# Performance work log

Measured on AMD Instinct MI355X. Metric: run time of the kernel, lower is better.

The kernel has to match this reference:

```python
import jax, jax.numpy as jnp
import numpy as np

N = 50000        # nodes
E = 800000       # edges (before self-loops)
F_IN = 256       # input feature dim
HID = 64         # hidden per head (concat=False -> head mean)
NCLS = 40        # classes
HEADS = 8
NEG_SLOPE = 0.2  # PyG GATConv default leaky_relu slope


def setup_inputs() -> dict:
    key = jax.random.key(0)
    ks = jax.random.split(key, 11)
    s = 0.1
    return {
        "x": jax.random.normal(ks[0], (N, F_IN), jnp.float32),
        "edge_index": jax.random.randint(ks[1], (2, E), 0, N, dtype=jnp.int64),
        "edge_attr": jax.random.uniform(ks[2], (E, 1), jnp.float32),
        "W0": jax.random.normal(ks[3], (HEADS * HID, F_IN), jnp.float32) * s,
        "a0s": jax.random.normal(ks[4], (HEADS, HID), jnp.float32) * s,
        "a0d": jax.random.normal(ks[5], (HEADS, HID), jnp.float32) * s,
        "b0": jnp.zeros((HID,), jnp.float32),
        "W2": jax.random.normal(ks[6], (HEADS * NCLS, HID), jnp.float32) * s,
        "a2s": jax.random.normal(ks[7], (HEADS, NCLS), jnp.float32) * s,
        "a2d": jax.random.normal(ks[8], (HEADS, NCLS), jnp.float32) * s,
        "b2": jnp.zeros((NCLS,), jnp.float32),
    }


def _gat_conv(x, src, dst, W, att_src, att_dst, bias, heads, out_c):
    # Linear: [N, in] @ [heads*out, in]^T -> [N, heads, out]
    h = (x @ W.T).reshape(N, heads, out_c)
    # Per-node attention logits, gathered per edge.
    a_s = jnp.einsum('nhc,hc->nh', h, att_src)
    a_d = jnp.einsum('nhc,hc->nh', h, att_dst)
    e = jax.nn.leaky_relu(a_s[src] + a_d[dst], NEG_SLOPE)  # [E, H]
    # Segment softmax over incoming edges of each destination node.
    m = jax.ops.segment_max(e, dst, num_segments=N)
    p = jnp.exp(e - m[dst])
    denom = jax.ops.segment_sum(p, dst, num_segments=N)
    alpha = p / (denom[dst] + 1e-16)
    # Weighted message scatter-sum: [E,H,C] -> [N,H,C]
    out = jax.ops.segment_sum(alpha[:, :, None] * h[src], dst, num_segments=N)
    # concat=False -> mean over heads, then bias.
    return out.mean(axis=1) + bias


def reference(x, edge_index, edge_attr, W0, a0s, a0d, b0, W2, a2s, a2d, b2):
    # edge_attr is unpacked by the torch forward but never used by GATConv.
    # PyG GATConv adds self-loops by default.
    loops = jnp.arange(N, dtype=edge_index.dtype)
    src = jnp.concatenate([edge_index[0], loops])
    dst = jnp.concatenate([edge_index[1], loops])
    h = jax.nn.relu(_gat_conv(x, src, dst, W0, a0s, a0d, b0, HEADS, HID))
    # dropout is identity in eval mode
    out = _gat_conv(h, src, dst, W2, a2s, a2d, b2, HEADS, NCLS)
    return jax.nn.log_softmax(out, axis=1)
```

## Files before the change

### kernel.cpp

```cpp
#include <hip/hip_runtime.h>
#include <hip/hip_bf16.h>
#include <math.h>


#define NEG_SLOPE 0.2f

typedef short v8s __attribute__((ext_vector_type(8)));
typedef float v4f __attribute__((ext_vector_type(4)));
typedef float v2f __attribute__((ext_vector_type(2)));
typedef unsigned short u16;
typedef unsigned int u32;
typedef unsigned char u8;

__device__ __forceinline__ u16 f2bf(float f) {
    union { float f; u32 u; } v; v.f = f;
    u32 r = v.u + 0x7fffu + ((v.u >> 16) & 1u);
    return (u16)(r >> 16);
}
__device__ __forceinline__ float lrelu_exp(float e) {
    e = (e > 0.f) ? e : NEG_SLOPE * e;
    return __expf(e);
}
__device__ __forceinline__ void dec8(uint2 r, float* h) {
    v2f a = __builtin_amdgcn_cvt_pk_f32_fp8(r.x, false);
    v2f b = __builtin_amdgcn_cvt_pk_f32_fp8(r.x, true);
    v2f c = __builtin_amdgcn_cvt_pk_f32_fp8(r.y, false);
    v2f d = __builtin_amdgcn_cvt_pk_f32_fp8(r.y, true);
    h[0] = a.x; h[1] = a.y; h[2] = b.x; h[3] = b.y;
    h[4] = c.x; h[5] = c.y; h[6] = d.x; h[7] = d.y;
}
__device__ __forceinline__ u8 enc8(float v) {
    u32 p = __builtin_amdgcn_cvt_pk_fp8_f32(v, v, 0u, false);
    return (u8)(p & 0xffu);
}


__global__ __launch_bounds__(256) void histcast_k(const int* __restrict__ ei, int* __restrict__ deg,
                                                  int E, int Nn, int NBh,
                                                  const float* __restrict__ x, u16* __restrict__ xb,
                                                  const float* __restrict__ W0, u16* __restrict__ W0b,
                                                  const float* __restrict__ W2, u16* __restrict__ W2b,
                                                  int nx, int n0c, int n2c) {
    int b = blockIdx.x;
    if (b < NBh) {
        int e = b * 256 + threadIdx.x;
        int ET = E + Nn;
        if (e >= ET) return;
        int d = (e < E) ? ei[E + e] : (e - E);
        atomicAdd(&deg[d], 1);
    } else {
        int i = ((b - NBh) * 256 + threadIdx.x) * 4;
        const float* in; u16* out;
        if (i < nx)            { in = x;  out = xb; }
        else if (i < nx + n0c) { in = W0; out = W0b; i -= nx; }
        else if (i < nx + n0c + n2c) { in = W2; out = W2b; i -= nx + n0c; }
        else return;
        float4 v = *reinterpret_cast<const float4*>(in + i);
        ushort4 o;
        o.x = f2bf(v.x); o.y = f2bf(v.y); o.z = f2bf(v.z); o.w = f2bf(v.w);
        *reinterpret_cast<ushort4*>(out + i) = o;
    }
}


__global__ __launch_bounds__(1024) void scanA_k(const int* __restrict__ deg, int* __restrict__ incl,
                                                int* __restrict__ bsum, int* __restrict__ dbin, int n) {
    __shared__ int wsum[16];
    __shared__ int dh[256];
    int t = threadIdx.x;
    if (t < 256) dh[t] = 0;
    int i = blockIdx.x * 1024 + t;
    int v = (i < n) ? deg[i] : 0;
    __syncthreads();
    if (i < n) atomicAdd(&dh[v < 255 ? v : 255], 1);
    int lane = t & 63, wid = t >> 6;
    int sv = v;
    for (int off = 1; off < 64; off <<= 1) {
        int u = __shfl_up(sv, off, 64);
        if (lane >= off) sv += u;
    }
    if (lane == 63) wsum[wid] = sv;
    __syncthreads();
    if (t < 16) {
        int w = wsum[t];
        for (int off = 1; off < 16; off <<= 1) {
            int u = __shfl_up(w, off, 64);
            if (t >= off) w += u;
        }
        wsum[t] = w;
    }
    if (t < 256 && dh[t] > 0) atomicAdd(&dbin[t], dh[t]);
    __syncthreads();
    int pre = (wid > 0) ? wsum[wid - 1] : 0;
    int inc = pre + sv;
    if (i < n) incl[i] = inc;
    if (t == 1023) bsum[blockIdx.x] = inc;
}


__global__ __launch_bounds__(256) void scanBC_k(const int* __restrict__ incl, const int* __restrict__ deg,
                                                const int* __restrict__ bsum, int* __restrict__ rowstart,
                                                int n, int B) {
    __shared__ int sb[65];
    int t = threadIdx.x;
    if (t < 64) {
        int v = (t < B) ? bsum[t] : 0;
        int sv = v;
        for (int off = 1; off < 64; off <<= 1) {
            int u = __shfl_up(sv, off, 64);
            if (t >= off) sv += u;
        }
        sb[t] = sv - v;
        if (t == 63) sb[64] = sv;
    }
    __syncthreads();
    int i = blockIdx.x * 256 + t;
    if (i < n) rowstart[i] = sb[i >> 10] + incl[i] - deg[i];
    if (i == 0) rowstart[n] = sb[64];
}


__global__ __launch_bounds__(256) void scatter_k(const int* __restrict__ ei,
                                                 const int* __restrict__ rowstart,
                                                 int* __restrict__ cursor,
                                                 int* __restrict__ srcs, int E, int Nn,
                                                 const int* __restrict__ deg,
                                                 const int* __restrict__ dbin,
                                                 int* __restrict__ dcur,
                                                 int* __restrict__ order) {
    int b = blockIdx.x, t = threadIdx.x;
    int e = b * 256 + t;
    int ET = E + Nn;
    if (e < ET) {
        int s, d;
        if (e < E) { s = ei[e]; d = ei[E + e]; }
        else       { s = e - E; d = e - E; }
        int pos = atomicAdd(&cursor[d], 1);
        srcs[rowstart[d] + pos] = s;
    }
    if (b * 256 < Nn) {
        __shared__ int ws4[4];
        __shared__ int sbase[256];
        __shared__ int lhist[256];
        __shared__ int lbase[256];
        lhist[t] = 0;
        int v = dbin[t];
        int lane = t & 63, wid = t >> 6;
        int sv = v;
        for (int off = 1; off < 64; off <<= 1) {
            int u = __shfl_up(sv, off, 64);
            if (lane >= off) sv += u;
        }
        if (lane == 63) ws4[wid] = sv;
        __syncthreads();
        int add = 0;
        for (int k = 0; k < wid; k++) add += ws4[k];
        sbase[t] = add + sv - v;
        __syncthreads();
        int i = b * 256 + t;
        int d = 0, rank = -1;
        if (i < Nn) {
            d = deg[i]; d = (d < 255) ? d : 255;
            rank = atomicAdd(&lhist[d], 1);
        }
        __syncthreads();
        int cnt = lhist[t];
        if (cnt > 0) lbase[t] = atomicAdd(&dcur[t], cnt);
        __syncthreads();
        if (i < Nn) order[Nn - 1 - (sbase[d] + lbase[d] + rank)] = i;
    }
}


template<int KK>
__global__ __launch_bounds__(256, 4) void gemm_mfma(const u16* __restrict__ Ab,
                                                    const u16* __restrict__ Bb,
                                                    u8* __restrict__ Cf, int M, int Nc,
                                                    const float* __restrict__ avs_vec,
                                                    const float* __restrict__ avd_vec,
                                                    float* as_out, float* ad_out) {
    constexpr int SB = KK + 8;
    constexpr int BBY = 64 * SB * 2;
    constexpr int LBY = (BBY > 10240) ? BBY : 10240;
    __shared__ __align__(16) u8 lds[LBY];
    u16* Bs = reinterpret_cast<u16*>(lds);
    const int t = threadIdx.x;

    const int lid = blockIdx.y * gridDim.x + blockIdx.x;
    const int GY = gridDim.y;
    const int r8 = lid & 7;
    const int rest = lid >> 3;
    const int row_blk = (rest / GY) * 8 + r8;
    const int col_blk = rest % GY;
    const int m0 = row_blk * 128;
    const int n0 = col_blk * 64;
    if (m0 >= M) return;

    const int w = t >> 6, lane = t & 63;
    const int wr = w * 32;
    const int q = lane >> 4, l16 = lane & 15;

    constexpr int NKC = KK / 32;
    constexpr int PF = (NKC < 4) ? NKC : 4;

    const u16* A0 = Ab + (size_t)(m0 + wr + l16) * KK + q * 8;
    const u16* A1 = A0 + (size_t)16 * KK;
    v8s pa0[PF], pa1[PF];
#pragma unroll
    for (int k = 0; k < PF; k++) {
        pa0[k] = *reinterpret_cast<const v8s*>(A0 + k * 32);
        pa1[k] = *reinterpret_cast<const v8s*>(A1 + k * 32);
    }

    constexpr int CH = KK / 8;
#pragma unroll
    for (int c = t; c < 64 * CH; c += 256) {
        int row = c / CH, ch = c % CH;
        int gn = n0 + row;
        uint4 vb = make_uint4(0u, 0u, 0u, 0u);
        if (gn < Nc) vb = *reinterpret_cast<const uint4*>(Bb + (size_t)gn * KK + ch * 8);
        *reinterpret_cast<uint4*>(&Bs[row * SB + ch * 8]) = vb;
    }
    __syncthreads();

    v4f acc[2][4];
#pragma unroll
    for (int i = 0; i < 2; i++)
#pragma unroll
        for (int j = 0; j < 4; j++) acc[i][j] = (v4f){0.f, 0.f, 0.f, 0.f};

#pragma unroll
    for (int kc = 0; kc < NKC; kc++) {
        v8s a0 = pa0[kc % PF];
        v8s a1 = pa1[kc % PF];
        if (kc + PF < NKC) {
            pa0[kc % PF] = *reinterpret_cast<const v8s*>(A0 + (kc + PF) * 32);
            pa1[kc % PF] = *reinterpret_cast<const v8s*>(A1 + (kc + PF) * 32);
        }
        v8s bf[4];
#pragma unroll
        for (int j = 0; j < 4; j++)
            bf[j] = *reinterpret_cast<const v8s*>(&Bs[(j * 16 + l16) * SB + kc * 32 + q * 8]);
#pragma unroll
        for (int j = 0; j < 4; j++) {
            acc[0][j] = __builtin_amdgcn_mfma_f32_16x16x32_bf16(a0, bf[j], acc[0][j], 0, 0, 0);
            acc[1][j] = __builtin_amdgcn_mfma_f32_16x16x32_bf16(a1, bf[j], acc[1][j], 0, 0, 0);
        }
    }

    const bool do_att = (as_out != nullptr);
    float avs[4], avd[4];
    if (do_att) {
#pragma unroll
        for (int j = 0; j < 4; j++) {
            avs[j] = avs_vec[n0 + j * 16 + l16];
            avd[j] = avd_vec[n0 + j * 16 + l16];
        }
    }
    const int head = n0 >> 6;

    __syncthreads();
    u8* Cs = lds;
#pragma unroll
    for (int i = 0; i < 2; i++) {
#pragma unroll
        for (int r = 0; r < 4; r++) {
            int row = wr + i * 16 + q * 4 + r;
#pragma unroll
            for (int j = 0; j < 4; j++)
                Cs[row * 80 + j * 16 + l16] = enc8(acc[i][j][r]);
            if (do_att) {
                int gm = m0 + row;
                float ps = 0.f, pd = 0.f;
#pragma unroll
                for (int j = 0; j < 4; j++) {
                    float v = acc[i][j][r];
                    ps = fmaf(v, avs[j], ps);
                    pd = fmaf(v, avd[j], pd);
                }
#pragma unroll
                for (int m = 1; m < 16; m <<= 1) {
                    ps += __shfl_xor(ps, m, 64);
                    pd += __shfl_xor(pd, m, 64);
                }
                if (l16 == 0 && gm < M) {
                    as_out[gm * 8 + head] = ps;
                    ad_out[gm * 8 + head] = pd;
                }
            }
        }
    }
    __syncthreads();
#pragma unroll
    for (int it = 0; it < 2; it++) {
        int idx = it * 256 + t;
        int row = idx >> 2, ch = idx & 3;
        int gm = m0 + row;
        if (gm < M)
            *reinterpret_cast<uint4*>(Cf + (size_t)gm * Nc + n0 + ch * 16) =
                *reinterpret_cast<const uint4*>(&Cs[row * 80 + ch * 16]);
    }
}


__global__ __launch_bounds__(256) void agg1_k(const u8* __restrict__ h1f,
                                              const float* __restrict__ as1, const float* __restrict__ ad1,
                                              const int* __restrict__ srcs, const int* __restrict__ rowstart,
                                              const int* __restrict__ order,
                                              const float* __restrict__ b0, u16* __restrict__ x1b, int Nn) {
    int wave = threadIdx.x >> 6, lane = threadIdx.x & 63;
    int gid = blockIdx.x * 4 + wave;
    if (gid >= Nn) return;
    int n = __builtin_amdgcn_readfirstlane(order[gid]);
    const int hl = lane >> 3;
    const float adl = ad1[n * 8 + hl];
    const u32 loff = (u32)lane * 8u;
    float acc[8] = {0, 0, 0, 0, 0, 0, 0, 0};
    float dsum = 0.f;
    int beg = rowstart[n], end = rowstart[n + 1];
    int i = beg;
    for (; i + 8 <= end; i += 8) {
        int s[8];
#pragma unroll
        for (int u = 0; u < 8; u++) s[u] = __builtin_amdgcn_readfirstlane(srcs[i + u]);
        uint2 rw[8];
#pragma unroll
        for (int u = 0; u < 8; u++) rw[u] = *reinterpret_cast<const uint2*>(h1f + ((u32)s[u] * 512u + loff));
        float eg[8];
#pragma unroll
        for (int u = 0; u < 8; u++) eg[u] = as1[(u32)s[u] * 8u + hl];
        float p[8];
#pragma unroll
        for (int u = 0; u < 8; u++) { p[u] = lrelu_exp(eg[u] + adl); dsum += p[u]; }
#pragma unroll
        for (int u = 0; u < 8; u++) {
            float hv[8];
            dec8(rw[u], hv);
#pragma unroll
            for (int j = 0; j < 8; j++) acc[j] = fmaf(p[u], hv[j], acc[j]);
        }
    }
    for (; i + 4 <= end; i += 4) {
        int s[4];
#pragma unroll
        for (int u = 0; u < 4; u++) s[u] = __builtin_amdgcn_readfirstlane(srcs[i + u]);
        uint2 rw[4];
#pragma unroll
        for (int u = 0; u < 4; u++) rw[u] = *reinterpret_cast<const uint2*>(h1f + ((u32)s[u] * 512u + loff));
        float eg[4];
#pragma unroll
        for (int u = 0; u < 4; u++) eg[u] = as1[(u32)s[u] * 8u + hl];
#pragma unroll
        for (int u = 0; u < 4; u++) {
            float p = lrelu_exp(eg[u] + adl);
            dsum += p;
            float hv[8];
            dec8(rw[u], hv);
#pragma unroll
            for (int j = 0; j < 8; j++) acc[j] = fmaf(p, hv[j], acc[j]);
        }
    }
    for (; i < end; i++) {
        int s = __builtin_amdgcn_readfirstlane(srcs[i]);
        uint2 raw = *reinterpret_cast<const uint2*>(h1f + ((u32)s * 512u + loff));
        float p = lrelu_exp(as1[(u32)s * 8u + hl] + adl);
        dsum += p;
        float hv[8];
        dec8(raw, hv);
#pragma unroll
        for (int j = 0; j < 8; j++) acc[j] = fmaf(p, hv[j], acc[j]);
    }
    float inv = 1.f / (dsum + 1e-16f);
    float r[8];
#pragma unroll
    for (int j = 0; j < 8; j++) r[j] = acc[j] * inv;
#pragma unroll
    for (int j = 0; j < 8; j++) {
        r[j] += __shfl_xor(r[j], 8, 64);
        r[j] += __shfl_xor(r[j], 16, 64);
        r[j] += __shfl_xor(r[j], 32, 64);
    }
    if (lane < 8) {
        u16 o[8];
#pragma unroll
        for (int j = 0; j < 8; j++) {
            float v = r[j] * 0.125f + b0[lane * 8 + j];
            o[j] = f2bf((v > 0.f) ? v : 0.f);
        }
        *reinterpret_cast<uint4*>(x1b + (size_t)n * 64 + lane * 8) =
            *reinterpret_cast<const uint4*>(o);
    }
}


__global__ __launch_bounds__(256) void att2_k(const u8* __restrict__ h2f,
                                              const float* __restrict__ a2s, const float* __restrict__ a2d,
                                              float* __restrict__ as2, float* __restrict__ ad2, int Nn) {
    int t = blockIdx.x * 256 + threadIdx.x;
    if (t >= Nn * 8) return;
    int n = t >> 3, h = t & 7;
    const u8* hr = h2f + (size_t)n * 320 + h * 40;
    float s1 = 0.f, s2 = 0.f;
#pragma unroll
    for (int b = 0; b < 5; b++) {
        uint2 raw = *reinterpret_cast<const uint2*>(hr + b * 8);
        float h8[8];
        dec8(raw, h8);
#pragma unroll
        for (int j = 0; j < 8; j++) {
            int c = h * 40 + b * 8 + j;
            s1 = fmaf(h8[j], a2s[c], s1);
            s2 = fmaf(h8[j], a2d[c], s2);
        }
    }
    as2[t] = s1;
    ad2[t] = s2;
}


__global__ __launch_bounds__(256) void agg2_k(const u8* __restrict__ h2f,
                                              const float* __restrict__ as2, const float* __restrict__ ad2,
                                              const int* __restrict__ srcs, const int* __restrict__ rowstart,
                                              const int* __restrict__ order,
                                              const float* __restrict__ b2, float* __restrict__ out, int Nn) {
    __shared__ float smem[4][320];
    int wave = threadIdx.x >> 6, lane = threadIdx.x & 63;
    int gid = blockIdx.x * 4 + wave;
    bool active = (gid < Nn);
    int n = 0;
    if (active) n = __builtin_amdgcn_readfirstlane(order[gid]);
    bool ld = active && (lane < 40);
    const int hl = lane / 5;
    float adl = ld ? ad2[n * 8 + hl] : 0.f;
    float acc[8] = {0, 0, 0, 0, 0, 0, 0, 0};
    float dsum = 0.f;
    if (ld) {
        const u32 loff = (u32)lane * 8u;
        int beg = rowstart[n], end = rowstart[n + 1];
        int i = beg;
        for (; i + 8 <= end; i += 8) {
            int s[8];
#pragma unroll
            for (int u = 0; u < 8; u++) s[u] = __builtin_amdgcn_readfirstlane(srcs[i + u]);
            uint2 rw[8];
#pragma unroll
            for (int u = 0; u < 8; u++) rw[u] = *reinterpret_cast<const uint2*>(h2f + ((u32)s[u] * 320u + loff));
            float eg[8];
#pragma unroll
            for (int u = 0; u < 8; u++) eg[u] = as2[(u32)s[u] * 8u + hl];
            float p[8];
#pragma unroll
            for (int u = 0; u < 8; u++) { p[u] = lrelu_exp(eg[u] + adl); dsum += p[u]; }
#pragma unroll
            for (int u = 0; u < 8; u++) {
                float hv[8];
                dec8(rw[u], hv);
#pragma unroll
                for (int j = 0; j < 8; j++) acc[j] = fmaf(p[u], hv[j], acc[j]);
            }
        }
        for (; i + 4 <= end; i += 4) {
            int s[4];
#pragma unroll
            for (int u = 0; u < 4; u++) s[u] = __builtin_amdgcn_readfirstlane(srcs[i + u]);
            uint2 rw[4];
#pragma unroll
            for (int u = 0; u < 4; u++) rw[u] = *reinterpret_cast<const uint2*>(h2f + ((u32)s[u] * 320u + loff));
            float eg[4];
#pragma unroll
            for (int u = 0; u < 4; u++) eg[u] = as2[(u32)s[u] * 8u + hl];
#pragma unroll
            for (int u = 0; u < 4; u++) {
                float p = lrelu_exp(eg[u] + adl);
                dsum += p;
                float hv[8];
                dec8(rw[u], hv);
#pragma unroll
                for (int j = 0; j < 8; j++) acc[j] = fmaf(p, hv[j], acc[j]);
            }
        }
        for (; i < end; i++) {
            int s = __builtin_amdgcn_readfirstlane(srcs[i]);
            uint2 raw = *reinterpret_cast<const uint2*>(h2f + ((u32)s * 320u + loff));
            float p = lrelu_exp(as2[(u32)s * 8u + hl] + adl);
            dsum += p;
            float hv[8];
            dec8(raw, hv);
#pragma unroll
            for (int j = 0; j < 8; j++) acc[j] = fmaf(p, hv[j], acc[j]);
        }
        float inv = 1.f / (dsum + 1e-16f);
#pragma unroll
        for (int j = 0; j < 8; j++) smem[wave][lane * 8 + j] = acc[j] * inv;
    }
    __syncthreads();
    if (active) {
        float v;
        if (lane < 40) {
            float ssum = 0.f;
#pragma unroll
            for (int h = 0; h < 8; h++) ssum += smem[wave][h * 40 + lane];
            v = ssum * 0.125f + b2[lane];
        } else {
            v = -INFINITY;
        }
        float m = v;
        for (int off = 32; off > 0; off >>= 1) m = fmaxf(m, __shfl_xor(m, off, 64));
        float ex = (lane < 40) ? __expf(v - m) : 0.f;
        float se = ex;
        for (int off = 32; off > 0; off >>= 1) se += __shfl_xor(se, off, 64);
        if (lane < 40) out[(size_t)n * 40 + lane] = v - m - __logf(se);
    }
}


extern "C" void kernel_launch(void* const* d_in, const int* in_sizes, int n_in,
                              void* d_out, int out_size, void* d_ws, size_t ws_size,
                              hipStream_t stream) {
    const float* x   = (const float*)d_in[0];
    const int*   ei  = (const int*)d_in[1];
    const float* W0  = (const float*)d_in[3];
    const float* a0s = (const float*)d_in[4];
    const float* a0d = (const float*)d_in[5];
    const float* b0  = (const float*)d_in[6];
    const float* W2  = (const float*)d_in[7];
    const float* a2s = (const float*)d_in[8];
    const float* a2d = (const float*)d_in[9];
    const float* b2  = (const float*)d_in[10];
    float* out = (float*)d_out;

    const int Nn = in_sizes[0] / 256;
    const int E  = in_sizes[1] / 2;
    const int ET = E + Nn;
    const int NB = (Nn + 1023) / 1024;

    size_t off = 0;
    auto carve = [&](size_t bytes) -> void* {
        void* p = (char*)d_ws + off;
        off += (bytes + 255) & ~(size_t)255;
        return p;
    };
    u16*   xb       = (u16*)carve((size_t)Nn * 256 * 2);
    u16*   W0b      = (u16*)carve((size_t)512 * 256 * 2);
    u16*   W2b      = (u16*)carve((size_t)320 * 64 * 2);
    u8*    h1f      = (u8*)carve((size_t)Nn * 512);
    u16*   x1b      = (u16*)carve((size_t)Nn * 64 * 2);
    u8*    h2f      = (u8*)carve((size_t)Nn * 320);
    float* as1      = (float*)carve((size_t)Nn * 8 * 4);
    float* ad1      = (float*)carve((size_t)Nn * 8 * 4);
    float* as2      = (float*)carve((size_t)Nn * 8 * 4);
    float* ad2      = (float*)carve((size_t)Nn * 8 * 4);
    int*   deg      = (int*)carve((size_t)Nn * 4);
    int*   cursor   = (int*)carve((size_t)Nn * 4);
    int*   dbin     = (int*)carve(256 * 4);
    int*   dcur     = (int*)carve(256 * 4);
    int*   rowstart = (int*)carve((size_t)(Nn + 1) * 4);
    int*   srcs     = (int*)carve((size_t)ET * 4);
    int*   incl     = (int*)carve((size_t)Nn * 4);
    int*   bsum     = (int*)carve(64 * 4);
    int*   order    = (int*)carve((size_t)Nn * 4);

    const size_t zlen = (size_t)((char*)rowstart - (char*)deg);
    hipMemsetAsync(deg, 0, zlen, stream);

    const int nx = Nn * 256, n0c = 512 * 256, n2c = 320 * 64;
    const int NBh = (ET + 255) / 256;
    const int NBc = ((nx + n0c + n2c) / 4 + 255) / 256;
    histcast_k<<<NBh + NBc, 256, 0, stream>>>(ei, deg, E, Nn, NBh,
                                              x, xb, W0, W0b, W2, W2b, nx, n0c, n2c);
    scanA_k<<<NB, 1024, 0, stream>>>(deg, incl, bsum, dbin, Nn);
    scanBC_k<<<(Nn + 255) / 256, 256, 0, stream>>>(incl, deg, bsum, rowstart, Nn, NB);
    scatter_k<<<(ET + 255) / 256, 256, 0, stream>>>(ei, rowstart, cursor, srcs, E, Nn,
                                                    deg, dbin, dcur, order);

    const int GXr = (Nn + 127) / 128;
    const int GX  = ((GXr + 7) / 8) * 8;

    gemm_mfma<256><<<dim3(GX, 8), 256, 0, stream>>>(
        xb, W0b, h1f, Nn, 512, a0s, a0d, as1, ad1);
    agg1_k<<<(Nn + 3) / 4, 256, 0, stream>>>(h1f, as1, ad1, srcs, rowstart, order, b0, x1b, Nn);

    gemm_mfma<64><<<dim3(GX, 5), 256, 0, stream>>>(
        x1b, W2b, h2f, Nn, 320, nullptr, nullptr, nullptr, nullptr);
    att2_k<<<(Nn * 8 + 255) / 256, 256, 0, stream>>>(h2f, a2s, a2d, as2, ad2, Nn);
    agg2_k<<<(Nn + 3) / 4, 256, 0, stream>>>(h2f, as2, ad2, srcs, rowstart, order, b2, out, Nn);
}
```

Before: 379.2 us.

## Split layer-1 features into channel chunks and aggregate per chunk

The first GEMM now writes its fp8 output in a chunked layout: 8 chunks, each holding 8 channels across all 8 heads, i.e. 64 bytes per node. Layer-1 aggregation launches 8 times as many blocks, one per node and channel chunk, so each gathered row is a contiguous 64-byte slab. Within a wave, 8 edges are processed in parallel across lane groups and then reduced with shuffles. The aim is to shrink the per-edge gather footprint, which may improve cache locality and parallelism, at the cost of recomputing the attention exponentials 8 times and reading the edge lists 8 times.

Result: slower. 544.6 us (+43.6%).

```diff
diff --git a/kernel.cpp b/kernel.cpp
--- a/kernel.cpp
+++ b/kernel.cpp
@@ -291,103 +291,89 @@
         }
     }
     __syncthreads();
-#pragma unroll
-    for (int it = 0; it < 2; it++) {
-        int idx = it * 256 + t;
-        int row = idx >> 2, ch = idx & 3;
-        int gm = m0 + row;
-        if (gm < M)
-            *reinterpret_cast<uint4*>(Cf + (size_t)gm * Nc + n0 + ch * 16) =
-                *reinterpret_cast<const uint4*>(&Cs[row * 80 + ch * 16]);
-    }
-}
-
-
-__global__ __launch_bounds__(256) void agg1_k(const u8* __restrict__ h1f,
+    if (do_att) {
+#pragma unroll
+        for (int it = 0; it < 4; it++) {
+            int idx = it * 256 + t;
+            int row = idx >> 3, c8 = idx & 7;
+            int gm = m0 + row;
+            if (gm < M)
+                *reinterpret_cast<uint2*>(Cf + (size_t)c8 * M * 64 + (size_t)gm * 64 + head * 8) =
+                    *reinterpret_cast<const uint2*>(&Cs[row * 80 + c8 * 8]);
+        }
+    } else {
+#pragma unroll
+        for (int it = 0; it < 2; it++) {
+            int idx = it * 256 + t;
+            int row = idx >> 2, ch = idx & 3;
+            int gm = m0 + row;
+            if (gm < M)
+                *reinterpret_cast<uint4*>(Cf + (size_t)gm * Nc + n0 + ch * 16) =
+                    *reinterpret_cast<const uint4*>(&Cs[row * 80 + ch * 16]);
+        }
+    }
+}
+
+
+__global__ __launch_bounds__(256) void agg1_k(const u8* __restrict__ h1c,
                                               const float* __restrict__ as1, const float* __restrict__ ad1,
                                               const int* __restrict__ srcs, const int* __restrict__ rowstart,
                                               const int* __restrict__ order,
                                               const float* __restrict__ b0, u16* __restrict__ x1b, int Nn) {
     int wave = threadIdx.x >> 6, lane = threadIdx.x & 63;
-    int gid = blockIdx.x * 4 + wave;
+    int lid = blockIdx.x;
+    int c8 = lid & 7, nc = lid >> 3;
+    int gid = nc * 4 + wave;
     if (gid >= Nn) return;
     int n = __builtin_amdgcn_readfirstlane(order[gid]);
-    const int hl = lane >> 3;
-    const float adl = ad1[n * 8 + hl];
-    const u32 loff = (u32)lane * 8u;
+    const int eg = lane >> 3;
+    const int h  = lane & 7;
+    const float adl = ad1[n * 8 + h];
+    const u8* base = h1c + (size_t)c8 * Nn * 64;
     float acc[8] = {0, 0, 0, 0, 0, 0, 0, 0};
     float dsum = 0.f;
     int beg = rowstart[n], end = rowstart[n + 1];
-    int i = beg;
-    for (; i + 8 <= end; i += 8) {
-        int s[8];
-#pragma unroll
-        for (int u = 0; u < 8; u++) s[u] = __builtin_amdgcn_readfirstlane(srcs[i + u]);
-        uint2 rw[8];
-#pragma unroll
-        for (int u = 0; u < 8; u++) rw[u] = *reinterpret_cast<const uint2*>(h1f + ((u32)s[u] * 512u + loff));
-        float eg[8];
-#pragma unroll
-        for (int u = 0; u < 8; u++) eg[u] = as1[(u32)s[u] * 8u + hl];
-        float p[8];
-#pragma unroll
-        for (int u = 0; u < 8; u++) { p[u] = lrelu_exp(eg[u] + adl); dsum += p[u]; }
-#pragma unroll
-        for (int u = 0; u < 8; u++) {
-            float hv[8];
-            dec8(rw[u], hv);
-#pragma unroll
-            for (int j = 0; j < 8; j++) acc[j] = fmaf(p[u], hv[j], acc[j]);
-        }
-    }
-    for (; i + 4 <= end; i += 4) {
-        int s[4];
-#pragma unroll
-        for (int u = 0; u < 4; u++) s[u] = __builtin_amdgcn_readfirstlane(srcs[i + u]);
-        uint2 rw[4];
-#pragma unroll
-        for (int u = 0; u < 4; u++) rw[u] = *reinterpret_cast<const uint2*>(h1f + ((u32)s[u] * 512u + loff));
-        float eg[4];
-#pragma unroll
-        for (int u = 0; u < 4; u++) eg[u] = as1[(u32)s[u] * 8u + hl];
-#pragma unroll
-        for (int u = 0; u < 4; u++) {
-            float p = lrelu_exp(eg[u] + adl);
-            dsum += p;
-            float hv[8];
-            dec8(rw[u], hv);
-#pragma unroll
-            for (int j = 0; j < 8; j++) acc[j] = fmaf(p, hv[j], acc[j]);
-        }
-    }
-    for (; i < end; i++) {
-        int s = __builtin_amdgcn_readfirstlane(srcs[i]);
-        uint2 raw = *reinterpret_cast<const uint2*>(h1f + ((u32)s * 512u + loff));
-        float p = lrelu_exp(as1[(u32)s * 8u + hl] + adl);
+    int sfb = srcs[beg];
+    for (int i0 = beg; i0 < end; i0 += 8) {
+        int i = i0 + eg;
+        bool act = (i < end);
+        int s = act ? srcs[i] : sfb;
+        uint2 raw = *reinterpret_cast<const uint2*>(base + (u32)s * 64u + h * 8u);
+        float e = as1[s * 8 + h] + adl;
+        float p = act ? lrelu_exp(e) : 0.f;
         dsum += p;
         float hv[8];
         dec8(raw, hv);
 #pragma unroll
         for (int j = 0; j < 8; j++) acc[j] = fmaf(p, hv[j], acc[j]);
     }
+#pragma unroll
+    for (int j = 0; j < 8; j++) {
+        acc[j] += __shfl_xor(acc[j], 8, 64);
+        acc[j] += __shfl_xor(acc[j], 16, 64);
+        acc[j] += __shfl_xor(acc[j], 32, 64);
+    }
+    dsum += __shfl_xor(dsum, 8, 64);
+    dsum += __shfl_xor(dsum, 16, 64);
+    dsum += __shfl_xor(dsum, 32, 64);
     float inv = 1.f / (dsum + 1e-16f);
     float r[8];
 #pragma unroll
     for (int j = 0; j < 8; j++) r[j] = acc[j] * inv;
 #pragma unroll
     for (int j = 0; j < 8; j++) {
-        r[j] += __shfl_xor(r[j], 8, 64);
-        r[j] += __shfl_xor(r[j], 16, 64);
-        r[j] += __shfl_xor(r[j], 32, 64);
-    }
-    if (lane < 8) {
+        r[j] += __shfl_xor(r[j], 1, 64);
+        r[j] += __shfl_xor(r[j], 2, 64);
+        r[j] += __shfl_xor(r[j], 4, 64);
+    }
+    if (lane == 0) {
         u16 o[8];
 #pragma unroll
         for (int j = 0; j < 8; j++) {
-            float v = r[j] * 0.125f + b0[lane * 8 + j];
+            float v = r[j] * 0.125f + b0[c8 * 8 + j];
             o[j] = f2bf((v > 0.f) ? v : 0.f);
         }
-        *reinterpret_cast<uint4*>(x1b + (size_t)n * 64 + lane * 8) =
+        *reinterpret_cast<uint4*>(x1b + (size_t)n * 64 + c8 * 8) =
             *reinterpret_cast<const uint4*>(o);
     }
 }
@@ -543,7 +529,7 @@
     u16*   xb       = (u16*)carve((size_t)Nn * 256 * 2);
     u16*   W0b      = (u16*)carve((size_t)512 * 256 * 2);
     u16*   W2b      = (u16*)carve((size_t)320 * 64 * 2);
-    u8*    h1f      = (u8*)carve((size_t)Nn * 512);
+    u8*    h1c      = (u8*)carve((size_t)Nn * 512);
     u16*   x1b      = (u16*)carve((size_t)Nn * 64 * 2);
     u8*    h2f      = (u8*)carve((size_t)Nn * 320);
     float* as1      = (float*)carve((size_t)Nn * 8 * 4);
@@ -577,8 +563,8 @@
     const int GX  = ((GXr + 7) / 8) * 8;
 
     gemm_mfma<256><<<dim3(GX, 8), 256, 0, stream>>>(
-        xb, W0b, h1f, Nn, 512, a0s, a0d, as1, ad1);
-    agg1_k<<<(Nn + 3) / 4, 256, 0, stream>>>(h1f, as1, ad1, srcs, rowstart, order, b0, x1b, Nn);
+        xb, W0b, h1c, Nn, 512, a0s, a0d, as1, ad1);
+    agg1_k<<<((Nn + 3) / 4) * 8, 256, 0, stream>>>(h1c, as1, ad1, srcs, rowstart, order, b0, x1b, Nn);
 
     gemm_mfma<64><<<dim3(GX, 5), 256, 0, stream>>>(
         x1b, W2b, h2f, Nn, 320, nullptr, nullptr, nullptr, nullptr);
```
